# Performance work log

Hardware: AMD Instinct MI355X
Metric: run time of the kernel (lower is better)

The kernel has to match this reference:

```python
import jax, jax.numpy as jnp
import numpy as np

EMB_D, N_SLOTS, KEY_D, N_ITER = 768, 8, 128, 5
ATTN_EPS = 1e-8
LN_EPS = 1e-5


def layer_norm(x, g, b):
    mu = jnp.mean(x, axis=-1, keepdims=True)
    var = jnp.mean(jnp.square(x - mu), axis=-1, keepdims=True)
    return (x - mu) * jax.lax.rsqrt(var + LN_EPS) * g + b


def xavier(key, shape):
    fan_in, fan_out = shape[-1], shape[-2] if len(shape) > 1 else shape[-1]
    a = float(np.sqrt(6.0 / (fan_in + fan_out)))
    return jax.random.uniform(key, shape, jnp.float32, -a, a)


def setup_inputs() -> dict:
    key = jax.random.key(0)
    ks = jax.random.split(key, 24)
    B, N = 128, 196
    k = KEY_D
    inp = {
        "features": jax.random.normal(ks[0], (B, N, EMB_D), jnp.float32),
        "slot_noise": jax.random.normal(ks[1], (B, N_SLOTS, k), jnp.float32),
        # LayerNorms
        "ln_in_g": jnp.ones((EMB_D,), jnp.float32), "ln_in_b": jnp.zeros((EMB_D,), jnp.float32),
        "ln_slot_g": jnp.ones((k,), jnp.float32), "ln_slot_b": jnp.zeros((k,), jnp.float32),
        "ln_out_g": jnp.ones((k,), jnp.float32), "ln_out_b": jnp.zeros((k,), jnp.float32),
        "ln_dec_g": jnp.ones((k,), jnp.float32), "ln_dec_b": jnp.zeros((k,), jnp.float32),
        # slot prior
        "mu": xavier(ks[2], (1, 1, k)),
        "log_sigma": xavier(ks[3], (1, 1, k)),
        # projections (torch Linear weight layout: [out, in])
        "Wk": xavier(ks[4], (k, EMB_D)),
        "Wq": xavier(ks[5], (k, k)),
        "Wv": xavier(ks[6], (k, EMB_D)),
        # GRUCell
        "W_ih": jax.random.uniform(ks[7], (3 * k, k), jnp.float32, -1.0/np.sqrt(k), 1.0/np.sqrt(k)),
        "W_hh": jax.random.uniform(ks[8], (3 * k, k), jnp.float32, -1.0/np.sqrt(k), 1.0/np.sqrt(k)),
        "b_ih": jnp.zeros((3 * k,), jnp.float32),
        "b_hh": jnp.zeros((3 * k,), jnp.float32),
        # slot MLP
        "mlp_W1": xavier(ks[9], (k, k)), "mlp_b1": jnp.zeros((k,), jnp.float32),
        "mlp_W2": xavier(ks[10], (k, k)), "mlp_b2": jnp.zeros((k,), jnp.float32),
        # decoder
        "dec_W1": xavier(ks[11], (2 * k, k)), "dec_b1": jnp.zeros((2 * k,), jnp.float32),
        "dec_W2": xavier(ks[12], (EMB_D, 2 * k)), "dec_b2": jnp.zeros((EMB_D,), jnp.float32),
        "dec_W3": xavier(ks[13], (EMB_D, EMB_D)), "dec_b3": jnp.zeros((EMB_D,), jnp.float32),
    }
    return inp


def gru_cell(x, h, W_ih, W_hh, b_ih, b_hh):
    gi = x @ W_ih.T + b_ih  # [*, 3k]
    gh = h @ W_hh.T + b_hh
    ir, iz, inn = jnp.split(gi, 3, axis=-1)
    hr, hz, hn = jnp.split(gh, 3, axis=-1)
    r = jax.nn.sigmoid(ir + hr)
    z = jax.nn.sigmoid(iz + hz)
    n = jnp.tanh(inn + r * hn)
    return (1.0 - z) * n + z * h


def reference(features, slot_noise, ln_in_g, ln_in_b, ln_slot_g, ln_slot_b,
              ln_out_g, ln_out_b, ln_dec_g, ln_dec_b, mu, log_sigma,
              Wk, Wq, Wv, W_ih, W_hh, b_ih, b_hh,
              mlp_W1, mlp_b1, mlp_W2, mlp_b2,
              dec_W1, dec_b1, dec_W2, dec_b2, dec_W3, dec_b3):
    feats_ln = layer_norm(features, ln_in_g, ln_in_b)  # [B,N,E]
    slots = slot_noise * jnp.exp(log_sigma) + mu       # [B,K,D]
    k_proj = (feats_ln @ Wk.T) * (KEY_D ** -0.5)       # [B,N,D]
    v_proj = feats_ln @ Wv.T                           # [B,N,D]

    attn_vis = None
    for _ in range(N_ITER):
        slots_prev = slots
        s_ln = layer_norm(slots, ln_slot_g, ln_slot_b)
        q = s_ln @ Wq.T                                # [B,K,D]
        logits = jnp.einsum('bnd,bkd->bnk', k_proj, q)
        attn_vis = jax.nn.softmax(logits, axis=-1)     # softmax over slots
        attn = attn_vis + ATTN_EPS
        attn = attn / jnp.sum(attn, axis=-2, keepdims=True)  # normalize over tokens
        updates = jnp.einsum('bnk,bnd->bkd', attn, v_proj)
        slots = gru_cell(updates, slots_prev, W_ih, W_hh, b_ih, b_hh)
        h = jax.nn.relu(layer_norm(slots, ln_out_g, ln_out_b) @ mlp_W1.T + mlp_b1)
        slots = slots + (h @ mlp_W2.T + mlp_b2)

    sf = layer_norm(slots, ln_dec_g, ln_dec_b)
    sf = jax.nn.relu(sf @ dec_W1.T + dec_b1)
    sf = jax.nn.relu(sf @ dec_W2.T + dec_b2)
    sf = sf @ dec_W3.T + dec_b3                        # [B,K,E]
    recon = jnp.einsum('bkd,bnk->bnd', sf, attn_vis)   # [B,N,E]
    recon_loss = jnp.mean(jnp.square(recon - features))
    return slots, attn_vis, recon_loss
```

## Files before the change

kernel.cpp:

```cpp
#include <hip/hip_runtime.h>
#include <hip/hip_bf16.h>
#include <math.h>

#define B_    128
#define N_    196
#define E_    768
#define K_    8
#define D_    128
#define BNR   (B_*N_)
#define ITERS 5

#define OFF_PART   0
#define OFF_SDEC   512
#define OFF_WBF    66048
#define OFF_KPBF   639488
#define OFF_VPTBF  2343424
#define OFF_ABF    4178432

typedef __attribute__((ext_vector_type(8))) short bf16x8;
typedef __attribute__((ext_vector_type(4))) float f32x4;

#define MFMA16(a, b, c) __builtin_amdgcn_mfma_f32_16x16x32_bf16(a, b, c, 0, 0, 0)

__device__ __forceinline__ float wave_red_sum64(float v) {
    #pragma unroll
    for (int o = 32; o > 0; o >>= 1) v += __shfl_xor(v, o);
    return v;
}

__device__ __forceinline__ unsigned short f2bf(float v) {
    union { float f; unsigned int u; } c; c.f = v;
    unsigned int u = c.u + 0x7fffu + ((c.u >> 16) & 1u);
    return (unsigned short)(u >> 16);
}

__device__ __forceinline__ void gl_lds16(const void* g, void* l) {
    __builtin_amdgcn_global_load_lds(
        (const __attribute__((address_space(1))) unsigned int*)g,
        (__attribute__((address_space(3))) unsigned int*)l, 16, 0, 0);
}

__device__ __forceinline__ int swz128(int row, int j) {
    return row * 128 + ((((j >> 3) ^ (row & 7))) << 3) + (j & 7);
}
__device__ __forceinline__ int swz256(int row, int j) {
    return row * 256 + ((((j >> 3) ^ (row & 7))) << 3) + (j & 7);
}
__device__ __forceinline__ bf16x8 ldA128(const unsigned short* base, int row, int kq, int ks) {
    int ch = (ks * 4 + kq) ^ (row & 7);
    return *(const bf16x8*)(base + row * 128 + ch * 8);
}
__device__ __forceinline__ bf16x8 ldA256(const unsigned short* base, int row, int kq, int ks) {
    int ch = (ks * 4 + kq) ^ (row & 7);
    return *(const bf16x8*)(base + row * 256 + ch * 8);
}
__device__ __forceinline__ bf16x8 ldW128(const unsigned short* W, int row, int ks, int kq) {
    return *(const bf16x8*)(W + (size_t)row * 128 + ks * 32 + kq * 8);
}

struct WCEnt { const float* s; unsigned short* d; int t0; };
struct WCArgs { WCEnt m[8]; };

__global__ __launch_bounds__(256) void prep_all_k(const float* __restrict__ Wq,
                                                  const float* __restrict__ Wk,
                                                  unsigned short* __restrict__ WMt,
                                                  WCArgs a,
                                                  unsigned short* __restrict__ kpb,
                                                  unsigned short* __restrict__ vpt) {
    __shared__ __align__(16) unsigned short Aq[128 * 128];
    __shared__ __align__(16) unsigned short Bk[128 * 128];
    int bid = blockIdx.x;
    int t = threadIdx.x;
    if (bid < 6) {
        const float s = 0.08838834764831845f;
        int e0 = bid * 128;
        for (int idx = t; idx < 16384; idx += 256) {
            int o = idx >> 7, c = idx & 127;
            Aq[swz128(c, o)] = f2bf(Wq[(size_t)o * 128 + c]);
            Bk[swz128(c, o)] = f2bf(Wk[(size_t)o * 768 + e0 + c] * s);
        }
        __syncthreads();
        int w = t >> 6, l = t & 63;
        int wr = w >> 1, wc = w & 1, fr = l & 15, kq = l >> 4;
        f32x4 acc[4][4];
        #pragma unroll
        for (int mi = 0; mi < 4; ++mi)
            #pragma unroll
            for (int nj = 0; nj < 4; ++nj) acc[mi][nj] = (f32x4){0.f, 0.f, 0.f, 0.f};
        #pragma unroll
        for (int ks = 0; ks < 4; ++ks) {
            bf16x8 af[4], bfr[4];
            #pragma unroll
            for (int mi = 0; mi < 4; ++mi) af[mi] = ldA128(Aq, wr * 64 + mi * 16 + fr, kq, ks);
            #pragma unroll
            for (int nj = 0; nj < 4; ++nj) bfr[nj] = ldA128(Bk, wc * 64 + nj * 16 + fr, kq, ks);
            #pragma unroll
            for (int mi = 0; mi < 4; ++mi)
                #pragma unroll
                for (int nj = 0; nj < 4; ++nj)
                    acc[mi][nj] = MFMA16(af[mi], bfr[nj], acc[mi][nj]);
        }
        #pragma unroll
        for (int mi = 0; mi < 4; ++mi) {
            int rowbase = wr * 64 + mi * 16 + kq * 4;
            #pragma unroll
            for (int nj = 0; nj < 4; ++nj) {
                int col = e0 + wc * 64 + nj * 16 + fr;
                #pragma unroll
                for (int r = 0; r < 4; ++r)
                    WMt[(size_t)(rowbase + r) * 768 + col] = f2bf(acc[mi][nj][r]);
            }
        }
    } else if (bid < 518) {
        int cbid = bid - 6, i = 0;
        #pragma unroll
        for (int j = 1; j < 8; ++j) if (cbid >= a.m[j].t0) i = j;
        int off = (cbid - a.m[i].t0) * 2048 + t * 8;
        const float* s = a.m[i].s + off;
        unsigned short* d = a.m[i].d + off;
        float4 v0 = *(const float4*)s, v1 = *(const float4*)(s + 4);
        ushort4 o0, o1;
        o0.x = f2bf(v0.x); o0.y = f2bf(v0.y); o0.z = f2bf(v0.z); o0.w = f2bf(v0.w);
        o1.x = f2bf(v1.x); o1.y = f2bf(v1.y); o1.z = f2bf(v1.z); o1.w = f2bf(v1.w);
        *(ushort4*)d = o0; *(ushort4*)(d + 4) = o1;
    } else {
        int i = (bid - 518) * 256 + t;
        ushort4 z = {0, 0, 0, 0};
        if (i < 49152) {
            int q = i * 4;
            int b = q / 1536, off = q - b * 1536;
            *(ushort4*)(kpb + ((size_t)b * 208 + 196) * 128 + off) = z;
        } else {
            int c = i - 49152;
            int bd = c / 7, cc = c - bd * 7;
            *(ushort4*)(vpt + (size_t)bd * 224 + 196 + cc * 4) = z;
        }
    }
}

__global__ __launch_bounds__(256) void ln_bf16_k(const float* __restrict__ f,
                                                 const float* __restrict__ g,
                                                 const float* __restrict__ bv,
                                                 unsigned short* __restrict__ out) {
    int wid = blockIdx.x * 4 + (threadIdx.x >> 6);
    int lane = threadIdx.x & 63;
    const float* row = f + (size_t)wid * E_;
    float4 x[3];
    float s = 0.f, s2 = 0.f;
    #pragma unroll
    for (int c = 0; c < 3; ++c) {
        x[c] = *(const float4*)(row + c * 256 + lane * 4);
        s  += x[c].x + x[c].y + x[c].z + x[c].w;
        s2 += x[c].x * x[c].x + x[c].y * x[c].y + x[c].z * x[c].z + x[c].w * x[c].w;
    }
    s  = wave_red_sum64(s);
    s2 = wave_red_sum64(s2);
    float m = s * (1.f / E_);
    float rs = rsqrtf(s2 * (1.f / E_) - m * m + 1e-5f);
    #pragma unroll
    for (int c = 0; c < 3; ++c) {
        float4 g4 = *(const float4*)(g + c * 256 + lane * 4);
        float4 b4 = *(const float4*)(bv + c * 256 + lane * 4);
        ushort4 o;
        o.x = f2bf((x[c].x - m) * rs * g4.x + b4.x);
        o.y = f2bf((x[c].y - m) * rs * g4.y + b4.y);
        o.z = f2bf((x[c].z - m) * rs * g4.z + b4.z);
        o.w = f2bf((x[c].w - m) * rs * g4.w + b4.w);
        *(ushort4*)(out + (size_t)wid * E_ + c * 256 + lane * 4) = o;
    }
}

__global__ __launch_bounds__(512) void mfma_proj_k(const unsigned short* __restrict__ Abf,
                                                   const unsigned short* __restrict__ WMt,
                                                   const unsigned short* __restrict__ Wv_bf,
                                                   unsigned short* __restrict__ kpq_bf,
                                                   unsigned short* __restrict__ vpT_bf) {
    __shared__ __align__(16) unsigned short As[128 * 64];
    __shared__ __align__(16) unsigned short Bs[256 * 64];
    const int t = threadIdx.x, w = t >> 6, l = t & 63;
    const int m0 = blockIdx.x * 128;
    const int wr = w >> 2, wc = w & 3;
    const int fr = l & 15, kq = l >> 4;
    f32x4 acc[4][4];
    #pragma unroll
    for (int mi = 0; mi < 4; ++mi)
        #pragma unroll
        for (int nj = 0; nj < 4; ++nj) acc[mi][nj] = (f32x4){0.f, 0.f, 0.f, 0.f};

    for (int ks = 0; ks < E_; ks += 64) {
        __syncthreads();
        #pragma unroll
        for (int j = 0; j < 2; ++j) {
            int ci = j * 512 + (w << 6) + l;
            int r = ci >> 3, c = ci & 7, cg = c ^ (r & 7);
            gl_lds16(Abf + (size_t)(m0 + r) * E_ + ks + cg * 8,
                     As + (size_t)(j * 512 + (w << 6)) * 8);
        }
        #pragma unroll
        for (int j = 0; j < 4; ++j) {
            int ci = j * 512 + (w << 6) + l;
            int r = ci >> 3, c = ci & 7, cg = c ^ (r & 7);
            const unsigned short* src = (r < 128)
                ? WMt   + (size_t)r * E_ + ks + cg * 8
                : Wv_bf + (size_t)(r - 128) * E_ + ks + cg * 8;
            gl_lds16(src, Bs + (size_t)(j * 512 + (w << 6)) * 8);
        }
        __syncthreads();
        #pragma unroll
        for (int kk = 0; kk < 2; ++kk) {
            bf16x8 af[4], bfr[4];
            #pragma unroll
            for (int mi = 0; mi < 4; ++mi) {
                int rr = wr * 64 + mi * 16 + fr;
                af[mi] = *(const bf16x8*)(As + rr * 64 + (((kk * 4 + kq) ^ (rr & 7))) * 8);
            }
            #pragma unroll
            for (int nj = 0; nj < 4; ++nj) {
                int rr = wc * 64 + nj * 16 + fr;
                bfr[nj] = *(const bf16x8*)(Bs + rr * 64 + (((kk * 4 + kq) ^ (rr & 7))) * 8);
            }
            #pragma unroll
            for (int mi = 0; mi < 4; ++mi)
                #pragma unroll
                for (int nj = 0; nj < 4; ++nj)
                    acc[mi][nj] = MFMA16(af[mi], bfr[nj], acc[mi][nj]);
        }
    }
    __syncthreads();
    if (wc < 2) {
        #pragma unroll
        for (int mi = 0; mi < 4; ++mi) {
            int rowbase = m0 + wr * 64 + mi * 16 + kq * 4;
            #pragma unroll
            for (int r = 0; r < 4; ++r) {
                int m = rowbase + r;
                int b = m / 196, rr = m - b * 196;
                size_t o = ((size_t)b * 208 + rr) * 128;
                #pragma unroll
                for (int nj = 0; nj < 4; ++nj)
                    kpq_bf[o + wc * 64 + nj * 16 + fr] = f2bf(acc[mi][nj][r]);
            }
        }
    } else {
        int dbase = (wc - 2) * 64;
        #pragma unroll
        for (int mi = 0; mi < 4; ++mi) {
            int tok = wr * 64 + mi * 16 + kq * 4;
            #pragma unroll
            for (int nj = 0; nj < 4; ++nj) {
                int d = dbase + nj * 16 + fr;
                ushort4 pk;
                pk.x = f2bf(acc[mi][nj][0]); pk.y = f2bf(acc[mi][nj][1]);
                pk.z = f2bf(acc[mi][nj][2]); pk.w = f2bf(acc[mi][nj][3]);
                *(ushort4*)(Bs + d * 128 + (tok ^ ((d & 7) << 3))) = pk;
            }
        }
    }
    __syncthreads();
    {
        int d = t >> 2, mg = t & 3;
        #pragma unroll
        for (int sc = 0; sc < 4; ++sc) {
            int mstart = mg * 32 + sc * 8;
            int cm = mstart >> 3;
            const unsigned short* src = Bs + d * 128 + ((cm ^ (d & 7)) << 3);
            int g0 = m0 + mstart;
            int b0 = g0 / 196, rr0 = g0 - b0 * 196;
            int b7 = (g0 + 7) / 196;
            if (b0 == b7) {
                unsigned short* dst = vpT_bf + ((size_t)b0 * 128 + d) * 224 + rr0;
                *(ushort4*)(dst)     = *(const ushort4*)(src);
                *(ushort4*)(dst + 4) = *(const ushort4*)(src + 4);
            } else {
                #pragma unroll
                for (int e = 0; e < 8; ++e) {
                    int g = g0 + e;
                    int bb = g / 196, rr = g - bb * 196;
                    vpT_bf[((size_t)bb * 128 + d) * 224 + rr] = src[e];
                }
            }
        }
    }
}

template<int KTOT, int EPI>
__global__ __launch_bounds__(256) void mfma_mlp_k(const unsigned short* __restrict__ A,
                                                  const unsigned short* __restrict__ Bw,
                                                  const float* __restrict__ bias,
                                                  unsigned short* __restrict__ out_bf,
                                                  float* __restrict__ out_f,
                                                  int ldN) {
    __shared__ __align__(16) unsigned short As[128 * 64];
    __shared__ __align__(16) unsigned short Bs[128 * 64];
    const int t = threadIdx.x, w = t >> 6, l = t & 63;
    const int m0 = blockIdx.x * 128;
    const int n0 = blockIdx.y * 128;
    const int wr = w >> 1, wc = w & 1;
    const int fr = l & 15, kq = l >> 4;
    f32x4 acc[4][4];
    #pragma unroll
    for (int mi = 0; mi < 4; ++mi)
        #pragma unroll
        for (int nj = 0; nj < 4; ++nj) acc[mi][nj] = (f32x4){0.f, 0.f, 0.f, 0.f};

    for (int ks = 0; ks < KTOT; ks += 64) {
        __syncthreads();
        #pragma unroll
        for (int j = 0; j < 4; ++j) {
            int ci = (w << 8) + (j << 6) + l;
            int r = ci >> 3, c = ci & 7;
            int cg = c ^ (r & 7);
            gl_lds16(A  + (size_t)(m0 + r) * KTOT + ks + cg * 8,
                     As + (size_t)((w << 8) + (j << 6)) * 8);
            gl_lds16(Bw + (size_t)(n0 + r) * KTOT + ks + cg * 8,
                     Bs + (size_t)((w << 8) + (j << 6)) * 8);
        }
        __syncthreads();
        #pragma unroll
        for (int kk = 0; kk < 2; ++kk) {
            bf16x8 af[4], bfr[4];
            int ch = (kk * 4 + kq) ^ (fr & 7);
            #pragma unroll
            for (int mi = 0; mi < 4; ++mi)
                af[mi] = *(const bf16x8*)(As + (wr * 64 + mi * 16 + fr) * 64 + ch * 8);
            #pragma unroll
            for (int nj = 0; nj < 4; ++nj)
                bfr[nj] = *(const bf16x8*)(Bs + (wc * 64 + nj * 16 + fr) * 64 + ch * 8);
            #pragma unroll
            for (int mi = 0; mi < 4; ++mi)
                #pragma unroll
                for (int nj = 0; nj < 4; ++nj)
                    acc[mi][nj] = MFMA16(af[mi], bfr[nj], acc[mi][nj]);
        }
    }
    #pragma unroll
    for (int mi = 0; mi < 4; ++mi) {
        int rowbase = m0 + wr * 64 + mi * 16 + kq * 4;
        #pragma unroll
        for (int nj = 0; nj < 4; ++nj) {
            int col = n0 + wc * 64 + nj * 16 + fr;
            float bc = bias[col];
            #pragma unroll
            for (int r = 0; r < 4; ++r) {
                float v = acc[mi][nj][r] + bc;
                if (EPI == 0)
                    out_bf[(size_t)(rowbase + r) * ldN + col] = f2bf(fmaxf(v, 0.f));
                else
                    out_f[(size_t)(rowbase + r) * ldN + col] = v;
            }
        }
    }
}

__global__ __launch_bounds__(512) void slot_iter_mfma(
    const float* __restrict__ noise,
    const float* __restrict__ lsg, const float* __restrict__ lsb,
    const float* __restrict__ log_, const float* __restrict__ lob,
    const float* __restrict__ ldg_, const float* __restrict__ ldb_,
    const float* __restrict__ mup, const float* __restrict__ lsig,
    const unsigned short* __restrict__ Wih_bf,
    const unsigned short* __restrict__ Whh_bf,
    const float* __restrict__ bih, const float* __restrict__ bhh,
    const unsigned short* __restrict__ W1_bf, const float* __restrict__ mb1,
    const unsigned short* __restrict__ W2_bf, const float* __restrict__ mb2,
    const unsigned short* __restrict__ kpq_bf,
    const unsigned short* __restrict__ vpT_bf,
    float* __restrict__ out_slots, float* __restrict__ out_attn,
    unsigned short* __restrict__ sdec_bf) {

    __shared__ float slots[8][128];
    __shared__ float colpart[8][8];
    __shared__ __align__(16) unsigned short sln_bf[2048];
    __shared__ __align__(16) unsigned short upd_bf[2048];
    __shared__ __align__(16) unsigned short slots_bf[2048];
    __shared__ __align__(16) unsigned short h_bf[2048];
    __shared__ __align__(16) unsigned short attnT_bf[4096];

    const int b = blockIdx.x, t = threadIdx.x;
    const int lane = t & 63, w = t >> 6;
    const int fr = lane & 15, kq = lane >> 4;

    for (int i = t; i < 2048; i += 512) {
        sln_bf[i] = 0; upd_bf[i] = 0; slots_bf[i] = 0; h_bf[i] = 0;
    }
    for (int i = t; i < 4096; i += 512) attnT_bf[i] = 0;

    for (int idx = t; idx < 1024; idx += 512) {
        int k = idx >> 7, d = idx & 127;
        float v = noise[(size_t)b * 1024 + idx] * expf(lsig[d]) + mup[d];
        slots[k][d] = v;
        slots_bf[swz128(k, d)] = f2bf(v);
    }

    bf16x8 kpq_r[2][4];
    #pragma unroll
    for (int p = 0; p < 2; ++p)
        #pragma unroll
        for (int ks = 0; ks < 4; ++ks) kpq_r[p][ks] = (bf16x8){0,0,0,0,0,0,0,0};
    #pragma unroll
    for (int p = 0; p < 2; ++p) {
        int tt = w + p * 8;
        if (tt <= 12) {
            const unsigned short* kpr = kpq_bf + ((size_t)b * 208 + tt * 16 + fr) * 128;
            #pragma unroll
            for (int ks = 0; ks < 4; ++ks)
                kpq_r[p][ks] = *(const bf16x8*)(kpr + ks * 32 + kq * 8);
        }
    }
    bf16x8 vpt_r[7];
    {
        const unsigned short* vpr = vpT_bf + ((size_t)b * 128 + w * 16 + fr) * 224;
        #pragma unroll
        for (int ks = 0; ks < 7; ++ks)
            vpt_r[ks] = *(const bf16x8*)(vpr + ks * 32 + kq * 8);
    }
    bf16x8 w1_r[4], w2_r[4];
    #pragma unroll
    for (int ks = 0; ks < 4; ++ks) {
        w1_r[ks] = ldW128(W1_bf, w * 16 + fr, ks, kq);
        w2_r[ks] = ldW128(W2_bf, w * 16 + fr, ks, kq);
    }
    __syncthreads();

    for (int it = 0; it < ITERS; ++it) {
        bool last = (it == ITERS - 1);
        {
            float x0 = slots[w][lane], x1 = slots[w][lane + 64];
            float s  = wave_red_sum64(x0 + x1);
            float s2 = wave_red_sum64(x0 * x0 + x1 * x1);
            float m = s * 0.0078125f;
            float rs = rsqrtf(s2 * 0.0078125f - m * m + 1e-5f);
            sln_bf[swz128(w, lane)]      = f2bf((x0 - m) * rs * lsg[lane]      + lsb[lane]);
            sln_bf[swz128(w, lane + 64)] = f2bf((x1 - m) * rs * lsg[lane + 64] + lsb[lane + 64]);
        }
        __syncthreads();
        {
            float cp = 0.f;
            #pragma unroll
            for (int p = 0; p < 2; ++p) {
                int tt = w + p * 8;
                if (tt <= 12) {
                    f32x4 acc = {0.f, 0.f, 0.f, 0.f};
                    #pragma unroll
                    for (int ks = 0; ks < 4; ++ks)
                        acc = MFMA16(kpq_r[p][ks], ldA128(sln_bf, fr, kq, ks), acc);
                    #pragma unroll
                    for (int r = 0; r < 4; ++r) {
                        float v = acc[r];
                        float mx = fmaxf(v, __shfl_xor(v, 1));
                        mx = fmaxf(mx, __shfl_xor(mx, 2));
                        mx = fmaxf(mx, __shfl_xor(mx, 4));
                        float e = expf(v - mx);
                        float sm = e;
                        sm += __shfl_xor(sm, 1); sm += __shfl_xor(sm, 2); sm += __shfl_xor(sm, 4);
                        float a = e / sm;
                        int tok = tt * 16 + kq * 4 + r;
                        bool valid = (tok < 196);
                        if (fr < 8 && valid) {
                            attnT_bf[swz256(fr, tok)] = f2bf(a);
                            if (last) out_attn[((size_t)b * 196 + tok) * 8 + fr] = a;
                        }
                        cp += valid ? a : 0.f;
                    }
                }
            }
            cp += __shfl_xor(cp, 16);
            cp += __shfl_xor(cp, 32);
            if (lane < 8) colpart[w][lane] = cp;
        }
        __syncthreads();
        {
            f32x4 acc = {0.f, 0.f, 0.f, 0.f};
            #pragma unroll
            for (int ks = 0; ks < 7; ++ks)
                acc = MFMA16(ldA256(attnT_bf, fr, kq, ks), vpt_r[ks], acc);
            if (kq < 2) {
                #pragma unroll
                for (int r = 0; r < 4; ++r) {
                    int k = kq * 4 + r;
                    float cs = colpart[0][k] + colpart[1][k] + colpart[2][k] + colpart[3][k]
                             + colpart[4][k] + colpart[5][k] + colpart[6][k] + colpart[7][k]
                             + 196.0f * 1e-8f;
                    upd_bf[swz128(k, w * 16 + fr)] = f2bf(acc[r] / cs);
                }
            }
        }
        __syncthreads();
        {
            f32x4 gi0 = {0,0,0,0}, gi1 = {0,0,0,0}, gi2 = {0,0,0,0};
            f32x4 gh0 = {0,0,0,0}, gh1 = {0,0,0,0}, gh2 = {0,0,0,0};
            #pragma unroll
            for (int ks = 0; ks < 4; ++ks) {
                bf16x8 au = ldA128(upd_bf,   fr, kq, ks);
                bf16x8 as = ldA128(slots_bf, fr, kq, ks);
                gi0 = MFMA16(au, ldW128(Wih_bf,       w * 16 + fr, ks, kq), gi0);
                gi1 = MFMA16(au, ldW128(Wih_bf, 128 + w * 16 + fr, ks, kq), gi1);
                gi2 = MFMA16(au, ldW128(Wih_bf, 256 + w * 16 + fr, ks, kq), gi2);
                gh0 = MFMA16(as, ldW128(Whh_bf,       w * 16 + fr, ks, kq), gh0);
                gh1 = MFMA16(as, ldW128(Whh_bf, 128 + w * 16 + fr, ks, kq), gh1);
                gh2 = MFMA16(as, ldW128(Whh_bf, 256 + w * 16 + fr, ks, kq), gh2);
            }
            if (kq < 2) {
                int d = w * 16 + fr;
                float bi0 = bih[d], bi1 = bih[128 + d], bi2 = bih[256 + d];
                float bh0 = bhh[d], bh1 = bhh[128 + d], bh2 = bhh[256 + d];
                #pragma unroll
                for (int r = 0; r < 4; ++r) {
                    int m = kq * 4 + r;
                    float rr = 1.f / (1.f + expf(-((gi0[r] + bi0) + (gh0[r] + bh0))));
                    float zz = 1.f / (1.f + expf(-((gi1[r] + bi1) + (gh1[r] + bh1))));
                    float nn = tanhf((gi2[r] + bi2) + rr * (gh2[r] + bh2));
                    float h = slots[m][d];
                    slots[m][d] = (1.f - zz) * nn + zz * h;
                }
            }
        }
        __syncthreads();
        {
            float x0 = slots[w][lane], x1 = slots[w][lane + 64];
            float s  = wave_red_sum64(x0 + x1);
            float s2 = wave_red_sum64(x0 * x0 + x1 * x1);
            float m = s * 0.0078125f;
            float rs = rsqrtf(s2 * 0.0078125f - m * m + 1e-5f);
            sln_bf[swz128(w, lane)]      = f2bf((x0 - m) * rs * log_[lane]      + lob[lane]);
            sln_bf[swz128(w, lane + 64)] = f2bf((x1 - m) * rs * log_[lane + 64] + lob[lane + 64]);
        }
        __syncthreads();
        {
            f32x4 acc = {0.f, 0.f, 0.f, 0.f};
            #pragma unroll
            for (int ks = 0; ks < 4; ++ks)
                acc = MFMA16(ldA128(sln_bf, fr, kq, ks), w1_r[ks], acc);
            if (kq < 2) {
                float b1 = mb1[w * 16 + fr];
                #pragma unroll
                for (int r = 0; r < 4; ++r)
                    h_bf[swz128(kq * 4 + r, w * 16 + fr)] = f2bf(fmaxf(acc[r] + b1, 0.f));
            }
        }
        __syncthreads();
        {
            f32x4 acc = {0.f, 0.f, 0.f, 0.f};
            #pragma unroll
            for (int ks = 0; ks < 4; ++ks)
                acc = MFMA16(ldA128(h_bf, fr, kq, ks), w2_r[ks], acc);
            if (kq < 2) {
                float b2 = mb2[w * 16 + fr];
                #pragma unroll
                for (int r = 0; r < 4; ++r) {
                    int m = kq * 4 + r, d = w * 16 + fr;
                    float v = slots[m][d] + acc[r] + b2;
                    slots[m][d] = v;
                    slots_bf[swz128(m, d)] = f2bf(v);
                }
            }
        }
        __syncthreads();
    }
    {
        float x0 = slots[w][lane], x1 = slots[w][lane + 64];
        out_slots[(size_t)b * 1024 + w * 128 + lane]      = x0;
        out_slots[(size_t)b * 1024 + w * 128 + lane + 64] = x1;
        float s  = wave_red_sum64(x0 + x1);
        float s2 = wave_red_sum64(x0 * x0 + x1 * x1);
        float m = s * 0.0078125f;
        float rs = rsqrtf(s2 * 0.0078125f - m * m + 1e-5f);
        sdec_bf[((size_t)b * 8 + w) * 128 + lane]      = f2bf((x0 - m) * rs * ldg_[lane]      + ldb_[lane]);
        sdec_bf[((size_t)b * 8 + w) * 128 + lane + 64] = f2bf((x1 - m) * rs * ldg_[lane + 64] + ldb_[lane + 64]);
    }
}

__global__ __launch_bounds__(256) void recon_loss_k(
    const float* __restrict__ feats, const float* __restrict__ attnv,
    const float* __restrict__ sf, float* __restrict__ partials) {

    __shared__ float sfl[8][768];
    __shared__ float al[49][8];
    __shared__ float wred[4];
    int b = blockIdx.x, qd = blockIdx.y, t = threadIdx.x;
    for (int idx = t; idx < 8 * 768; idx += 256)
        ((float*)sfl)[idx] = sf[(size_t)b * 8 * 768 + idx];
    int n0 = qd * 49;
    for (int idx = t; idx < 49 * 8; idx += 256)
        ((float*)al)[idx] = attnv[((size_t)b * N_ + n0) * 8 + idx];
    __syncthreads();
    float acc = 0.f;
    for (int nl = 0; nl < 49; ++nl) {
        float a0 = al[nl][0], a1 = al[nl][1], a2 = al[nl][2], a3 = al[nl][3];
        float a4 = al[nl][4], a5 = al[nl][5], a6 = al[nl][6], a7 = al[nl][7];
        const float* frow = feats + ((size_t)(b * N_ + n0 + nl)) * E_;
        for (int c = t; c < E_; c += 256) {
            float r = sfl[0][c]*a0 + sfl[1][c]*a1 + sfl[2][c]*a2 + sfl[3][c]*a3
                    + sfl[4][c]*a4 + sfl[5][c]*a5 + sfl[6][c]*a6 + sfl[7][c]*a7;
            float d = r - frow[c];
            acc += d * d;
        }
    }
    acc = wave_red_sum64(acc);
    int lane = t & 63, w = t >> 6;
    if (lane == 0) wred[w] = acc;
    __syncthreads();
    if (t == 0) partials[b * 4 + qd] = wred[0] + wred[1] + wred[2] + wred[3];
}

__global__ __launch_bounds__(512) void loss_final_k(const float* __restrict__ partials,
                                                    float* __restrict__ out) {
    __shared__ float wred[8];
    int t = threadIdx.x;
    float v = partials[t];
    v = wave_red_sum64(v);
    if ((t & 63) == 0) wred[t >> 6] = v;
    __syncthreads();
    if (t == 0) {
        float s = 0.f;
        #pragma unroll
        for (int i = 0; i < 8; ++i) s += wred[i];
        out[0] = s / (float)(B_ * N_ * E_);
    }
}

extern "C" void kernel_launch(void* const* d_in, const int* in_sizes, int n_in,
                              void* d_out, int out_size, void* d_ws, size_t ws_size,
                              hipStream_t stream) {
    (void)in_sizes; (void)n_in; (void)out_size; (void)ws_size;
    const float* feats     = (const float*)d_in[0];
    const float* noise     = (const float*)d_in[1];
    const float* ln_in_g   = (const float*)d_in[2];
    const float* ln_in_b   = (const float*)d_in[3];
    const float* ln_slot_g = (const float*)d_in[4];
    const float* ln_slot_b = (const float*)d_in[5];
    const float* ln_out_g  = (const float*)d_in[6];
    const float* ln_out_b  = (const float*)d_in[7];
    const float* ln_dec_g  = (const float*)d_in[8];
    const float* ln_dec_b  = (const float*)d_in[9];
    const float* mu        = (const float*)d_in[10];
    const float* log_sigma = (const float*)d_in[11];
    const float* Wk        = (const float*)d_in[12];
    const float* Wq        = (const float*)d_in[13];
    const float* Wv        = (const float*)d_in[14];
    const float* W_ih      = (const float*)d_in[15];
    const float* W_hh      = (const float*)d_in[16];
    const float* b_ih      = (const float*)d_in[17];
    const float* b_hh      = (const float*)d_in[18];
    const float* mlp_W1    = (const float*)d_in[19];
    const float* mlp_b1    = (const float*)d_in[20];
    const float* mlp_W2    = (const float*)d_in[21];
    const float* mlp_b2    = (const float*)d_in[22];
    const float* dec_W1    = (const float*)d_in[23];
    const float* dec_b1    = (const float*)d_in[24];
    const float* dec_W2    = (const float*)d_in[25];
    const float* dec_b2    = (const float*)d_in[26];
    const float* dec_W3    = (const float*)d_in[27];
    const float* dec_b3    = (const float*)d_in[28];

    float* ws    = (float*)d_ws;
    float* parts = ws + OFF_PART;
    unsigned short* sdec_bf = (unsigned short*)(ws + OFF_SDEC);
    unsigned short* Wbase   = (unsigned short*)(ws + OFF_WBF);
    unsigned short* Wv_bf   = Wbase;
    unsigned short* Wih_bf  = Wbase + 98304;
    unsigned short* Whh_bf  = Wbase + 147456;
    unsigned short* W1_bf   = Wbase + 196608;
    unsigned short* W2_bf   = Wbase + 212992;
    unsigned short* dW1_bf  = Wbase + 229376;
    unsigned short* dW2_bf  = Wbase + 262144;
    unsigned short* dW3_bf  = Wbase + 458752;
    unsigned short* WMt     = Wbase + 1048576;
    unsigned short* kpq_bf  = (unsigned short*)(ws + OFF_KPBF);
    unsigned short* vpT_bf  = (unsigned short*)(ws + OFF_VPTBF);
    unsigned short* Abf     = (unsigned short*)(ws + OFF_ABF);
    float*          sf      = ws + OFF_ABF;
    unsigned short* h1_bf   = (unsigned short*)(ws + OFF_ABF + 786432);
    unsigned short* h2_bf   = (unsigned short*)(ws + OFF_ABF + 786432 + 131072);

    float* out_slots = (float*)d_out;
    float* out_attn  = out_slots + 131072;
    float* out_loss  = out_slots + 331776;

    WCArgs wa;
    wa.m[0] = {Wv,     Wv_bf,  0};
    wa.m[1] = {W_ih,   Wih_bf, 48};
    wa.m[2] = {W_hh,   Whh_bf, 72};
    wa.m[3] = {mlp_W1, W1_bf,  96};
    wa.m[4] = {mlp_W2, W2_bf,  104};
    wa.m[5] = {dec_W1, dW1_bf, 112};
    wa.m[6] = {dec_W2, dW2_bf, 128};
    wa.m[7] = {dec_W3, dW3_bf, 224};
    prep_all_k<<<1158, 256, 0, stream>>>(Wq, Wk, WMt, wa, kpq_bf, vpT_bf);

    ln_bf16_k<<<BNR / 4, 256, 0, stream>>>(feats, ln_in_g, ln_in_b, Abf);
    mfma_proj_k<<<BNR / 128, 512, 0, stream>>>(Abf, WMt, Wv_bf, kpq_bf, vpT_bf);

    slot_iter_mfma<<<B_, 512, 0, stream>>>(noise, ln_slot_g, ln_slot_b, ln_out_g, ln_out_b,
                                           ln_dec_g, ln_dec_b, mu, log_sigma,
                                           Wih_bf, Whh_bf, b_ih, b_hh,
                                           W1_bf, mlp_b1, W2_bf, mlp_b2, kpq_bf, vpT_bf,
                                           out_slots, out_attn, sdec_bf);

    mfma_mlp_k<128, 0><<<dim3(8, 2), 256, 0, stream>>>(sdec_bf, dW1_bf, dec_b1, h1_bf, nullptr, 256);
    mfma_mlp_k<256, 0><<<dim3(8, 6), 256, 0, stream>>>(h1_bf,  dW2_bf, dec_b2, h2_bf, nullptr, 768);
    mfma_mlp_k<768, 1><<<dim3(8, 6), 256, 0, stream>>>(h2_bf,  dW3_bf, dec_b3, nullptr, sf, 768);

    recon_loss_k<<<dim3(B_, 4), 256, 0, stream>>>(feats, out_attn, sf, parts);
    loss_final_k<<<1, 512, 0, stream>>>(parts, out_loss);
}
```

Measured before the change: 206.1 us.

## Fuse input LayerNorm into projection GEMM and stop caching operands in registers

Removes the standalone LayerNorm kernel and its bf16 intermediate buffer. The projection GEMM now computes per-row mean and rstd itself and normalizes fp32 features while staging the A tile into LDS. This drops one kernel launch and a full write-then-read of the normalized activations, but the features are read twice and the async global-to-LDS copy for A becomes synchronous register loads. Separately, the slot-iteration kernel no longer holds kproj, vprojT and the MLP weight fragments in registers; it reloads them from global memory on every iteration, which lowers register pressure at the cost of repeated loads.

```diff
diff --git a/kernel.cpp b/kernel.cpp
--- a/kernel.cpp
+++ b/kernel.cpp
@@ -15,7 +15,7 @@
 #define OFF_WBF    66048
 #define OFF_KPBF   639488
 #define OFF_VPTBF  2343424
-#define OFF_ABF    4178432
+#define OFF_SF     4178432
 
 typedef __attribute__((ext_vector_type(8))) short bf16x8;
 typedef __attribute__((ext_vector_type(4))) float f32x4;
@@ -138,63 +138,72 @@
     }
 }
 
-__global__ __launch_bounds__(256) void ln_bf16_k(const float* __restrict__ f,
-                                                 const float* __restrict__ g,
-                                                 const float* __restrict__ bv,
-                                                 unsigned short* __restrict__ out) {
-    int wid = blockIdx.x * 4 + (threadIdx.x >> 6);
-    int lane = threadIdx.x & 63;
-    const float* row = f + (size_t)wid * E_;
-    float4 x[3];
-    float s = 0.f, s2 = 0.f;
-    #pragma unroll
-    for (int c = 0; c < 3; ++c) {
-        x[c] = *(const float4*)(row + c * 256 + lane * 4);
-        s  += x[c].x + x[c].y + x[c].z + x[c].w;
-        s2 += x[c].x * x[c].x + x[c].y * x[c].y + x[c].z * x[c].z + x[c].w * x[c].w;
-    }
-    s  = wave_red_sum64(s);
-    s2 = wave_red_sum64(s2);
-    float m = s * (1.f / E_);
-    float rs = rsqrtf(s2 * (1.f / E_) - m * m + 1e-5f);
-    #pragma unroll
-    for (int c = 0; c < 3; ++c) {
-        float4 g4 = *(const float4*)(g + c * 256 + lane * 4);
-        float4 b4 = *(const float4*)(bv + c * 256 + lane * 4);
-        ushort4 o;
-        o.x = f2bf((x[c].x - m) * rs * g4.x + b4.x);
-        o.y = f2bf((x[c].y - m) * rs * g4.y + b4.y);
-        o.z = f2bf((x[c].z - m) * rs * g4.z + b4.z);
-        o.w = f2bf((x[c].w - m) * rs * g4.w + b4.w);
-        *(ushort4*)(out + (size_t)wid * E_ + c * 256 + lane * 4) = o;
-    }
-}
-
-__global__ __launch_bounds__(512) void mfma_proj_k(const unsigned short* __restrict__ Abf,
+__global__ __launch_bounds__(512) void mfma_proj_k(const float* __restrict__ feats,
+                                                   const float* __restrict__ lg,
+                                                   const float* __restrict__ lb,
                                                    const unsigned short* __restrict__ WMt,
                                                    const unsigned short* __restrict__ Wv_bf,
                                                    unsigned short* __restrict__ kpq_bf,
                                                    unsigned short* __restrict__ vpT_bf) {
     __shared__ __align__(16) unsigned short As[128 * 64];
     __shared__ __align__(16) unsigned short Bs[256 * 64];
+    __shared__ float smu[128], srs[128];
     const int t = threadIdx.x, w = t >> 6, l = t & 63;
     const int m0 = blockIdx.x * 128;
     const int wr = w >> 2, wc = w & 3;
     const int fr = l & 15, kq = l >> 4;
+
+    for (int i = 0; i < 16; ++i) {
+        int r = w * 16 + i;
+        const float* row = feats + (size_t)(m0 + r) * E_;
+        float s = 0.f, s2 = 0.f;
+        #pragma unroll
+        for (int c = 0; c < 3; ++c) {
+            float4 x = *(const float4*)(row + c * 256 + l * 4);
+            s  += x.x + x.y + x.z + x.w;
+            s2 += x.x * x.x + x.y * x.y + x.z * x.z + x.w * x.w;
+        }
+        s  = wave_red_sum64(s);
+        s2 = wave_red_sum64(s2);
+        if (l == 0) {
+            float m = s * (1.f / E_);
+            smu[r] = m;
+            srs[r] = rsqrtf(s2 * (1.f / E_) - m * m + 1e-5f);
+        }
+    }
+
     f32x4 acc[4][4];
     #pragma unroll
     for (int mi = 0; mi < 4; ++mi)
         #pragma unroll
         for (int nj = 0; nj < 4; ++nj) acc[mi][nj] = (f32x4){0.f, 0.f, 0.f, 0.f};
+    __syncthreads();
 
     for (int ks = 0; ks < E_; ks += 64) {
-        __syncthreads();
+        if (ks) __syncthreads();
         #pragma unroll
         for (int j = 0; j < 2; ++j) {
-            int ci = j * 512 + (w << 6) + l;
+            int ci = j * 512 + t;
             int r = ci >> 3, c = ci & 7, cg = c ^ (r & 7);
-            gl_lds16(Abf + (size_t)(m0 + r) * E_ + ks + cg * 8,
-                     As + (size_t)(j * 512 + (w << 6)) * 8);
+            const float* src = feats + (size_t)(m0 + r) * E_ + ks + cg * 8;
+            float mu = smu[r], rs = srs[r];
+            float4 x0 = *(const float4*)src;
+            float4 x1 = *(const float4*)(src + 4);
+            float4 g0 = *(const float4*)(lg + ks + cg * 8);
+            float4 g1 = *(const float4*)(lg + ks + cg * 8 + 4);
+            float4 b0 = *(const float4*)(lb + ks + cg * 8);
+            float4 b1 = *(const float4*)(lb + ks + cg * 8 + 4);
+            ushort4 o0, o1;
+            o0.x = f2bf((x0.x - mu) * rs * g0.x + b0.x);
+            o0.y = f2bf((x0.y - mu) * rs * g0.y + b0.y);
+            o0.z = f2bf((x0.z - mu) * rs * g0.z + b0.z);
+            o0.w = f2bf((x0.w - mu) * rs * g0.w + b0.w);
+            o1.x = f2bf((x1.x - mu) * rs * g1.x + b1.x);
+            o1.y = f2bf((x1.y - mu) * rs * g1.y + b1.y);
+            o1.z = f2bf((x1.z - mu) * rs * g1.z + b1.z);
+            o1.w = f2bf((x1.w - mu) * rs * g1.w + b1.w);
+            *(ushort4*)(As + ci * 8)     = o0;
+            *(ushort4*)(As + ci * 8 + 4) = o1;
         }
         #pragma unroll
         for (int j = 0; j < 4; ++j) {
@@ -391,35 +400,6 @@
         slots[k][d] = v;
         slots_bf[swz128(k, d)] = f2bf(v);
     }
-
-    bf16x8 kpq_r[2][4];
-    #pragma unroll
-    for (int p = 0; p < 2; ++p)
-        #pragma unroll
-        for (int ks = 0; ks < 4; ++ks) kpq_r[p][ks] = (bf16x8){0,0,0,0,0,0,0,0};
-    #pragma unroll
-    for (int p = 0; p < 2; ++p) {
-        int tt = w + p * 8;
-        if (tt <= 12) {
-            const unsigned short* kpr = kpq_bf + ((size_t)b * 208 + tt * 16 + fr) * 128;
-            #pragma unroll
-            for (int ks = 0; ks < 4; ++ks)
-                kpq_r[p][ks] = *(const bf16x8*)(kpr + ks * 32 + kq * 8);
-        }
-    }
-    bf16x8 vpt_r[7];
-    {
-        const unsigned short* vpr = vpT_bf + ((size_t)b * 128 + w * 16 + fr) * 224;
-        #pragma unroll
-        for (int ks = 0; ks < 7; ++ks)
-            vpt_r[ks] = *(const bf16x8*)(vpr + ks * 32 + kq * 8);
-    }
-    bf16x8 w1_r[4], w2_r[4];
-    #pragma unroll
-    for (int ks = 0; ks < 4; ++ks) {
-        w1_r[ks] = ldW128(W1_bf, w * 16 + fr, ks, kq);
-        w2_r[ks] = ldW128(W2_bf, w * 16 + fr, ks, kq);
-    }
     __syncthreads();
 
     for (int it = 0; it < ITERS; ++it) {
@@ -441,9 +421,11 @@
                 int tt = w + p * 8;
                 if (tt <= 12) {
                     f32x4 acc = {0.f, 0.f, 0.f, 0.f};
+                    const unsigned short* kpr = kpq_bf + ((size_t)b * 208 + tt * 16 + fr) * 128;
                     #pragma unroll
                     for (int ks = 0; ks < 4; ++ks)
-                        acc = MFMA16(kpq_r[p][ks], ldA128(sln_bf, fr, kq, ks), acc);
+                        acc = MFMA16(*(const bf16x8*)(kpr + ks * 32 + kq * 8),
+                                     ldA128(sln_bf, fr, kq, ks), acc);
                     #pragma unroll
                     for (int r = 0; r < 4; ++r) {
                         float v = acc[r];
@@ -471,9 +453,11 @@
         __syncthreads();
         {
             f32x4 acc = {0.f, 0.f, 0.f, 0.f};
+            const unsigned short* vpr = vpT_bf + ((size_t)b * 128 + w * 16 + fr) * 224;
             #pragma unroll
             for (int ks = 0; ks < 7; ++ks)
-                acc = MFMA16(ldA256(attnT_bf, fr, kq, ks), vpt_r[ks], acc);
+                acc = MFMA16(ldA256(attnT_bf, fr, kq, ks),
+                             *(const bf16x8*)(vpr + ks * 32 + kq * 8), acc);
             if (kq < 2) {
                 #pragma unroll
                 for (int r = 0; r < 4; ++r) {
@@ -530,7 +514,7 @@
             f32x4 acc = {0.f, 0.f, 0.f, 0.f};
             #pragma unroll
             for (int ks = 0; ks < 4; ++ks)
-                acc = MFMA16(ldA128(sln_bf, fr, kq, ks), w1_r[ks], acc);
+                acc = MFMA16(ldA128(sln_bf, fr, kq, ks), ldW128(W1_bf, w * 16 + fr, ks, kq), acc);
             if (kq < 2) {
                 float b1 = mb1[w * 16 + fr];
                 #pragma unroll
@@ -543,7 +527,7 @@
             f32x4 acc = {0.f, 0.f, 0.f, 0.f};
             #pragma unroll
             for (int ks = 0; ks < 4; ++ks)
-                acc = MFMA16(ldA128(h_bf, fr, kq, ks), w2_r[ks], acc);
+                acc = MFMA16(ldA128(h_bf, fr, kq, ks), ldW128(W2_bf, w * 16 + fr, ks, kq), acc);
             if (kq < 2) {
                 float b2 = mb2[w * 16 + fr];
                 #pragma unroll
@@ -668,10 +652,9 @@
     unsigned short* WMt     = Wbase + 1048576;
     unsigned short* kpq_bf  = (unsigned short*)(ws + OFF_KPBF);
     unsigned short* vpT_bf  = (unsigned short*)(ws + OFF_VPTBF);
-    unsigned short* Abf     = (unsigned short*)(ws + OFF_ABF);
-    float*          sf      = ws + OFF_ABF;
-    unsigned short* h1_bf   = (unsigned short*)(ws + OFF_ABF + 786432);
-    unsigned short* h2_bf   = (unsigned short*)(ws + OFF_ABF + 786432 + 131072);
+    float*          sf      = ws + OFF_SF;
+    unsigned short* h1_bf   = (unsigned short*)(ws + OFF_SF + 786432);
+    unsigned short* h2_bf   = (unsigned short*)(ws + OFF_SF + 786432 + 131072);
 
     float* out_slots = (float*)d_out;
     float* out_attn  = out_slots + 131072;
@@ -688,8 +671,8 @@
     wa.m[7] = {dec_W3, dW3_bf, 224};
     prep_all_k<<<1158, 256, 0, stream>>>(Wq, Wk, WMt, wa, kpq_bf, vpT_bf);
 
-    ln_bf16_k<<<BNR / 4, 256, 0, stream>>>(feats, ln_in_g, ln_in_b, Abf);
-    mfma_proj_k<<<BNR / 128, 512, 0, stream>>>(Abf, WMt, Wv_bf, kpq_bf, vpT_bf);
+    mfma_proj_k<<<BNR / 128, 512, 0, stream>>>(feats, ln_in_g, ln_in_b,
+                                               WMt, Wv_bf, kpq_bf, vpT_bf);
 
     slot_iter_mfma<<<B_, 512, 0, stream>>>(noise, ln_slot_g, ln_slot_b, ln_out_g, ln_out_b,
                                            ln_dec_g, ln_dec_b, mu, log_sigma,
```

New measurement: 202.4 us (median of 2 runs). Within noise of the previous version (-1.8%).
